# Optimization experiments

Measured on AMD Instinct MI355X. Metric: run time of the kernel, lower is better.

Reference implementation:

```python
import jax, jax.numpy as jnp
import numpy as np

NUM_HEADS = 8
NUM_POINTS = 9


def _bilinear_sample(img, gx, gy):
    """grid_sample, mode=bilinear, padding=zeros, align_corners=True.
    img: (B, C, H, W); gx, gy: (B, M) pixel coords. Returns (B, C, M)."""
    Bc, C, H, W = img.shape
    imgf = img.reshape(Bc, C, H * W)
    x0 = jnp.floor(gx)
    y0 = jnp.floor(gy)
    wx1 = gx - x0
    wy1 = gy - y0

    def corner(xi, yi, w):
        valid = (xi >= 0) & (xi < W) & (yi >= 0) & (yi < H)
        xi_c = jnp.clip(xi, 0, W - 1).astype(jnp.int32)
        yi_c = jnp.clip(yi, 0, H - 1).astype(jnp.int32)
        idx = yi_c * W + xi_c  # (B, M)
        g = jax.vmap(lambda im, ix: im[:, ix])(imgf, idx)  # (B, C, M)
        return g * (w * valid)[:, None, :]

    return (corner(x0, y0, (1 - wx1) * (1 - wy1))
            + corner(x0 + 1, y0, wx1 * (1 - wy1))
            + corner(x0, y0 + 1, (1 - wx1) * wy1)
            + corner(x0 + 1, y0 + 1, wx1 * wy1))


def setup_inputs() -> dict:
    key = jax.random.key(0)
    ks = jax.random.split(key, 6)
    B, Hp, Wp, T, D = 4, 64, 64, 3, 256
    N = Hp * Wp
    Hh, P = NUM_HEADS, NUM_POINTS
    x = jax.random.normal(ks[0], (B, N, T, D), dtype=jnp.float32)
    # offset/attn projections: small random (orig inits them to 0, which is degenerate for testing)
    W_off = jax.random.normal(ks[1], (D, Hh * P * 2), dtype=jnp.float32) * 0.01
    b_off = jnp.zeros((Hh * P * 2,), dtype=jnp.float32)
    W_attn = jax.random.normal(ks[2], (D, Hh * P), dtype=jnp.float32) * 0.01
    b_attn = jnp.zeros((Hh * P,), dtype=jnp.float32)
    W_v = jax.random.normal(ks[3], (D, D), dtype=jnp.float32) * 0.02
    b_v = jnp.zeros((D,), dtype=jnp.float32)
    W_o = jax.random.normal(ks[4], (D, D), dtype=jnp.float32) * 0.02
    b_o = jnp.zeros((D,), dtype=jnp.float32)
    return {"x": x, "W_off": W_off, "b_off": b_off, "W_attn": W_attn,
            "b_attn": b_attn, "W_v": W_v, "b_v": b_v, "W_o": W_o,
            "b_o": b_o, "Hp": Hp, "Wp": Wp}


def reference(x, W_off, b_off, W_attn, b_attn, W_v, b_v, W_o, b_o, Hp, Wp):
    B, N, T, D = x.shape
    Hh, P = NUM_HEADS, NUM_POINTS
    dh = D // Hh

    query = x[:, :, T // 2]  # (B, N, D) middle frame
    offset = (query @ W_off + b_off).reshape(B, N, Hh, P, 2)
    attn = jax.nn.softmax((query @ W_attn + b_attn).reshape(B, N, Hh, P), axis=-1)

    # reference points in [-1, 1], xy order (x = width coord)
    gh, gw = jnp.meshgrid(jnp.arange(Hp, dtype=jnp.float32),
                          jnp.arange(Wp, dtype=jnp.float32), indexing='ij')
    ref = jnp.stack([gw, gh], axis=-1).reshape(N, 2)
    ref = ref / jnp.asarray([Wp - 1, Hp - 1], dtype=jnp.float32) * 2 - 1

    loc = ref[None, :, None, None, :] + offset  # (B, N, H, P, 2) normalized

    value = (x @ W_v + b_v).reshape(B, N, T, Hh, dh)
    # (B, H, T, dh, N) -> (B*H*T, dh, Hp, Wp)
    val = jnp.transpose(value, (0, 3, 2, 4, 1)).reshape(B * Hh * T, dh, Hp, Wp)

    # per-(b,h) grid, shared across frames; fold T into batch of the sampler
    grid = jnp.transpose(loc, (0, 2, 1, 3, 4))  # (B, H, N, P, 2)
    grid = jnp.broadcast_to(grid[:, :, None], (B, Hh, T, N, P, 2))
    grid = grid.reshape(B * Hh * T, N * P, 2)
    gx = (grid[..., 0] + 1) * 0.5 * (Wp - 1)
    gy = (grid[..., 1] + 1) * 0.5 * (Hp - 1)

    sampled = _bilinear_sample(val, gx, gy)  # (B*H*T, dh, N*P)
    sampled = sampled.reshape(B, Hh, T, dh, N, P)

    # weighted sum over points, summed over frames
    out = jnp.einsum('bhtdnp,bnhp->bnhd', sampled, attn).reshape(B, N, D)
    return out @ W_o + b_o
```

## Files before the change

kernel.cpp:

```cpp
#include <hip/hip_runtime.h>
#include <hip/hip_bf16.h>


#define NH_ 8
#define DH_ 32
#define MM_ 16384

typedef __attribute__((ext_vector_type(8))) _Float16 f16x8;
typedef __attribute__((ext_vector_type(4))) _Float16 f16x4;
typedef __attribute__((ext_vector_type(4))) float f32x4;

struct HL { _Float16 h, l; };
static __device__ __forceinline__ HL fsplit(float f) {
  HL r;
  r.h = (_Float16)f;
  r.l = (_Float16)(f - (float)r.h);
  return r;
}

__global__ __launch_bounds__(256) void prep(
    const float* __restrict__ x,
    const float* __restrict__ W_off, const float* __restrict__ W_attn,
    const float* __restrict__ W_v, const float* __restrict__ W_o,
    const float* __restrict__ b_off, const float* __restrict__ b_attn,
    _Float16* __restrict__ ash, _Float16* __restrict__ asl,
    _Float16* __restrict__ xmh, _Float16* __restrict__ xml,
    _Float16* __restrict__ wv, _Float16* __restrict__ wch,
    _Float16* __restrict__ wcl, _Float16* __restrict__ wo,
    float* __restrict__ bcat) {
  const int bid = blockIdx.x, t = threadIdx.x;
  if (bid < 4096) {
    const int gid = bid * 256 + t;
    const int row = gid >> 6, c4 = (gid & 63) * 4;
    const float* xr = x + (size_t)row * 768 + c4;
    float4 a0 = *(const float4*)xr;
    float4 a1 = *(const float4*)(xr + 256);
    float4 a2 = *(const float4*)(xr + 512);
    float s[4] = {a0.x + a1.x + a2.x, a0.y + a1.y + a2.y,
                  a0.z + a1.z + a2.z, a0.w + a1.w + a2.w};
    float m[4] = {a1.x, a1.y, a1.z, a1.w};
    f16x4 shv, slv, mhv, mlv;
#pragma unroll
    for (int j = 0; j < 4; ++j) {
      HL sj = fsplit(s[j]);
      shv[j] = sj.h; slv[j] = sj.l;
      HL mj = fsplit(m[j]);
      mhv[j] = mj.h; mlv[j] = mj.l;
    }
    const size_t o = (size_t)row * 256 + c4;
    *(f16x4*)(ash + o) = shv;  *(f16x4*)(asl + o) = slv;
    *(f16x4*)(xmh + o) = mhv;  *(f16x4*)(xml + o) = mlv;
  } else {
    const int n = bid - 4096;
    wv[n * 256 + t] = (_Float16)W_v[(size_t)t * 256 + n];
    wo[n * 256 + t] = (_Float16)W_o[(size_t)t * 256 + n];
    if (n < 216) {
      float v = (n < 144) ? W_off[(size_t)t * 144 + n] : W_attn[(size_t)t * 72 + (n - 144)];
      HL w = fsplit(v);
      wch[n * 256 + t] = w.h; wcl[n * 256 + t] = w.l;
    }
    if (n == 0 && t < 216) bcat[t] = (t < 144) ? b_off[t] : b_attn[t - 144];
  }
}

__global__ __launch_bounds__(256, 4) void mgemm01(
    const _Float16* __restrict__ Ahi, const _Float16* __restrict__ Alo,
    const _Float16* __restrict__ Xmh, const _Float16* __restrict__ Xml,
    const _Float16* __restrict__ Wv, const _Float16* __restrict__ Wch,
    const _Float16* __restrict__ Wcl,
    const float* __restrict__ b_v, const float* __restrict__ bcat,
    _Float16* __restrict__ valsum, float* __restrict__ proj) {
  __shared__ _Float16 Ah[64][64], Al[64][64], Bh[64][64], Bl[64][64];
  const int bid = blockIdx.x;
  const int flat = (bid & 7) * 256 + (bid >> 3);
  const int m0 = (flat >> 3) * 64;
  const int yy = flat & 7;
  const int mode1 = yy >= 4;
  const int n0 = (yy & 3) * 64;
  const int tid = threadIdx.x, wid = tid >> 6, lane = tid & 63;
  const int am = (wid >> 1) * 32, bn = (wid & 1) * 32;
  const int fr = lane & 15, kg = lane >> 4;
  const _Float16* Ahs = mode1 ? Xmh : Ahi;
  const _Float16* Als = mode1 ? Xml : Alo;
  const _Float16* Bhs = mode1 ? Wch : Wv;

  const int r0s = tid >> 3, c0s = tid & 7;
  const int r1s = r0s + 32;
  const int d0s = r0s * 64 + ((c0s ^ (r0s & 7)) * 8);
  const int d1s = r1s * 64 + ((c0s ^ (r1s & 7)) * 8);

  f32x4 acc[2][2];
#pragma unroll
  for (int i = 0; i < 2; ++i)
#pragma unroll
    for (int j = 0; j < 2; ++j) acc[i][j] = (f32x4)(0.f);

  f16x8 pah[2], pal[2], pbh[2], pbl[2];

#define LOADT01(k0)                                                          \
  {                                                                          \
    size_t a0 = (size_t)(m0 + r0s) * 256 + (k0) + c0s * 8;                   \
    size_t a1 = (size_t)(m0 + r1s) * 256 + (k0) + c0s * 8;                   \
    pah[0] = *(const f16x8*)(Ahs + a0); pal[0] = *(const f16x8*)(Als + a0);  \
    pah[1] = *(const f16x8*)(Ahs + a1); pal[1] = *(const f16x8*)(Als + a1);  \
    int nr0 = n0 + r0s, nr1 = n0 + r1s;                                      \
    size_t b0 = (size_t)nr0 * 256 + (k0) + c0s * 8;                          \
    size_t b1 = (size_t)nr1 * 256 + (k0) + c0s * 8;                          \
    if (!mode1 || nr0 < 216) pbh[0] = *(const f16x8*)(Bhs + b0);             \
    else pbh[0] = (f16x8)(_Float16)0.f;                                      \
    if (!mode1 || nr1 < 216) pbh[1] = *(const f16x8*)(Bhs + b1);             \
    else pbh[1] = (f16x8)(_Float16)0.f;                                      \
    if (mode1) {                                                             \
      pbl[0] = (nr0 < 216) ? *(const f16x8*)(Wcl + b0) : (f16x8)(_Float16)0.f;\
      pbl[1] = (nr1 < 216) ? *(const f16x8*)(Wcl + b1) : (f16x8)(_Float16)0.f;\
    }                                                                        \
  }

#define WRITET()                                                             \
  {                                                                          \
    *(f16x8*)(&Ah[0][0] + d0s) = pah[0]; *(f16x8*)(&Al[0][0] + d0s) = pal[0];\
    *(f16x8*)(&Ah[0][0] + d1s) = pah[1]; *(f16x8*)(&Al[0][0] + d1s) = pal[1];\
    *(f16x8*)(&Bh[0][0] + d0s) = pbh[0]; *(f16x8*)(&Bh[0][0] + d1s) = pbh[1];\
    if (mode1) {                                                             \
      *(f16x8*)(&Bl[0][0] + d0s) = pbl[0]; *(f16x8*)(&Bl[0][0] + d1s) = pbl[1];\
    }                                                                        \
  }

#define COMPUTET()                                                           \
  _Pragma("unroll")                                                          \
  for (int ks = 0; ks < 2; ++ks) {                                           \
    const int kc = ks * 4 + kg;                                              \
    f16x8 ah[2], al[2], bh[2];                                               \
    _Pragma("unroll")                                                        \
    for (int mi = 0; mi < 2; ++mi) {                                         \
      int m = am + mi * 16 + fr;                                             \
      int o = m * 64 + ((kc ^ (m & 7)) * 8);                                 \
      ah[mi] = *(const f16x8*)(&Ah[0][0] + o);                               \
      al[mi] = *(const f16x8*)(&Al[0][0] + o);                               \
    }                                                                        \
    _Pragma("unroll")                                                        \
    for (int ni = 0; ni < 2; ++ni) {                                         \
      int nn = bn + ni * 16 + fr;                                            \
      int o = nn * 64 + ((kc ^ (nn & 7)) * 8);                               \
      bh[ni] = *(const f16x8*)(&Bh[0][0] + o);                               \
      _Pragma("unroll")                                                      \
      for (int mi = 0; mi < 2; ++mi) {                                       \
        acc[mi][ni] = __builtin_amdgcn_mfma_f32_16x16x32_f16(ah[mi], bh[ni], acc[mi][ni], 0, 0, 0);\
        acc[mi][ni] = __builtin_amdgcn_mfma_f32_16x16x32_f16(al[mi], bh[ni], acc[mi][ni], 0, 0, 0);\
      }                                                                      \
      if (mode1) {                                                           \
        f16x8 bl = *(const f16x8*)(&Bl[0][0] + o);                           \
        _Pragma("unroll")                                                    \
        for (int mi = 0; mi < 2; ++mi)                                       \
          acc[mi][ni] = __builtin_amdgcn_mfma_f32_16x16x32_f16(ah[mi], bl, acc[mi][ni], 0, 0, 0);\
      }                                                                      \
    }                                                                        \
  }

  LOADT01(0);
  WRITET();
  __syncthreads();
#pragma unroll
  for (int t = 0; t < 4; ++t) {
    if (t < 3) LOADT01((t + 1) * 64);
    COMPUTET();
    __syncthreads();
    if (t < 3) { WRITET(); __syncthreads(); }
  }

  const int ro = kg * 4;
#pragma unroll
  for (int mi = 0; mi < 2; ++mi)
#pragma unroll
    for (int ni = 0; ni < 2; ++ni) {
      int col = n0 + bn + ni * 16 + fr;
      if (mode1 && col >= 216) continue;
      int rowb = m0 + am + mi * 16 + ro;
      float bv = mode1 ? bcat[col] : b_v[col] * 3.f;
#pragma unroll
      for (int r = 0; r < 4; ++r) {
        int grow = rowb + r;
        float v = acc[mi][ni][r] + bv;
        if (mode1) {
          proj[(size_t)grow * 216 + col] = v;
        } else {
          int b = grow >> 12, nn2 = grow & 4095;
          int h = col >> 5, d = col & 31;
          valsum[(((size_t)(b * NH_ + h) << 12) + nn2) * DH_ + d] = (_Float16)v;
        }
      }
    }
#undef LOADT01
#undef WRITET
#undef COMPUTET
}

__global__ __launch_bounds__(256, 4) void mgemm2(
    const _Float16* __restrict__ Ahi, const _Float16* __restrict__ Alo,
    const _Float16* __restrict__ Bhs,
    const float* __restrict__ bias, float* __restrict__ Cout) {
  __shared__ _Float16 Ah[64][64], Al[64][64], Bh[64][64];
  const int bid = blockIdx.x;
  const int flat = (bid & 7) * 128 + (bid >> 3);
  const int m0 = (flat >> 2) * 64;
  const int n0 = (flat & 3) * 64;
  const int tid = threadIdx.x, wid = tid >> 6, lane = tid & 63;
  const int am = (wid >> 1) * 32, bn = (wid & 1) * 32;
  const int fr = lane & 15, kg = lane >> 4;

  const int r0s = tid >> 3, c0s = tid & 7;
  const int r1s = r0s + 32;
  const int d0s = r0s * 64 + ((c0s ^ (r0s & 7)) * 8);
  const int d1s = r1s * 64 + ((c0s ^ (r1s & 7)) * 8);

  f32x4 acc[2][2];
#pragma unroll
  for (int i = 0; i < 2; ++i)
#pragma unroll
    for (int j = 0; j < 2; ++j) acc[i][j] = (f32x4)(0.f);

  f16x8 pah[2], pal[2], pbh[2];

#define LOADT2(k0)                                                           \
  {                                                                          \
    size_t a0 = (size_t)(m0 + r0s) * 256 + (k0) + c0s * 8;                   \
    size_t a1 = (size_t)(m0 + r1s) * 256 + (k0) + c0s * 8;                   \
    pah[0] = *(const f16x8*)(Ahi + a0); pal[0] = *(const f16x8*)(Alo + a0);  \
    pah[1] = *(const f16x8*)(Ahi + a1); pal[1] = *(const f16x8*)(Alo + a1);  \
    size_t b0 = (size_t)(n0 + r0s) * 256 + (k0) + c0s * 8;                   \
    size_t b1 = (size_t)(n0 + r1s) * 256 + (k0) + c0s * 8;                   \
    pbh[0] = *(const f16x8*)(Bhs + b0); pbh[1] = *(const f16x8*)(Bhs + b1);  \
  }

#define WRITET2()                                                            \
  {                                                                          \
    *(f16x8*)(&Ah[0][0] + d0s) = pah[0]; *(f16x8*)(&Al[0][0] + d0s) = pal[0];\
    *(f16x8*)(&Ah[0][0] + d1s) = pah[1]; *(f16x8*)(&Al[0][0] + d1s) = pal[1];\
    *(f16x8*)(&Bh[0][0] + d0s) = pbh[0]; *(f16x8*)(&Bh[0][0] + d1s) = pbh[1];\
  }

#define COMPUTET2()                                                          \
  _Pragma("unroll")                                                          \
  for (int ks = 0; ks < 2; ++ks) {                                           \
    const int kc = ks * 4 + kg;                                              \
    f16x8 ah[2], al[2], bh[2];                                               \
    _Pragma("unroll")                                                        \
    for (int mi = 0; mi < 2; ++mi) {                                         \
      int m = am + mi * 16 + fr;                                             \
      int o = m * 64 + ((kc ^ (m & 7)) * 8);                                 \
      ah[mi] = *(const f16x8*)(&Ah[0][0] + o);                               \
      al[mi] = *(const f16x8*)(&Al[0][0] + o);                               \
    }                                                                        \
    _Pragma("unroll")                                                        \
    for (int ni = 0; ni < 2; ++ni) {                                         \
      int nn = bn + ni * 16 + fr;                                            \
      int o = nn * 64 + ((kc ^ (nn & 7)) * 8);                               \
      bh[ni] = *(const f16x8*)(&Bh[0][0] + o);                               \
    }                                                                        \
    _Pragma("unroll")                                                        \
    for (int mi = 0; mi < 2; ++mi)                                           \
      _Pragma("unroll")                                                      \
      for (int ni = 0; ni < 2; ++ni) {                                       \
        acc[mi][ni] = __builtin_amdgcn_mfma_f32_16x16x32_f16(ah[mi], bh[ni], acc[mi][ni], 0, 0, 0);\
        acc[mi][ni] = __builtin_amdgcn_mfma_f32_16x16x32_f16(al[mi], bh[ni], acc[mi][ni], 0, 0, 0);\
      }                                                                      \
  }

  LOADT2(0);
  WRITET2();
  __syncthreads();
#pragma unroll
  for (int t = 0; t < 4; ++t) {
    if (t < 3) LOADT2((t + 1) * 64);
    COMPUTET2();
    __syncthreads();
    if (t < 3) { WRITET2(); __syncthreads(); }
  }

  const int ro = kg * 4;
#pragma unroll
  for (int mi = 0; mi < 2; ++mi)
#pragma unroll
    for (int ni = 0; ni < 2; ++ni) {
      int col = n0 + bn + ni * 16 + fr;
      int rowb = m0 + am + mi * 16 + ro;
      float bv = bias[col];
#pragma unroll
      for (int r = 0; r < 4; ++r)
        Cout[(size_t)(rowb + r) * 256 + col] = acc[mi][ni][r] + bv;
    }
#undef LOADT2
#undef WRITET2
#undef COMPUTET2
}

struct IW { int idx; float w; };

__global__ __launch_bounds__(256) void sample4(const _Float16* __restrict__ valsum,
                                               const float* __restrict__ proj,
                                               _Float16* __restrict__ ihi,
                                               _Float16* __restrict__ ilo) {
  const int bid = blockIdx.x;
  const int wv = threadIdx.x >> 6;
  const int lane = threadIdx.x & 63;
  const int row = ((bid & 7) << 11) + ((bid >> 3) << 2) + wv;
  const int b = row >> 12, n = row & 4095;

  __shared__ IW cwi[4][72][4];
  __shared__ float sap[4][76];

  const float* pr = proj + (size_t)row * 216;
  if (lane < 8) {
    const float* pa = pr + 144 + lane * 9;
    float lg[9], mx = -1e30f;
#pragma unroll
    for (int p = 0; p < 9; ++p) { lg[p] = pa[p]; mx = fmaxf(mx, lg[p]); }
    float s = 0.f;
#pragma unroll
    for (int p = 0; p < 9; ++p) { lg[p] = __expf(lg[p] - mx); s += lg[p]; }
    float inv = 1.f / s;
#pragma unroll
    for (int p = 0; p < 9; ++p) sap[wv][lane * 9 + p] = lg[p] * inv;
  }
  __syncthreads();
  for (int e = lane; e < 72; e += 64) {
    float ox = pr[e * 2], oy = pr[e * 2 + 1];
    float gx = (float)(n & 63) + ox * 31.5f;
    float gy = (float)(n >> 6) + oy * 31.5f;
    float fx0 = floorf(gx), fy0 = floorf(gy);
    float wx1 = gx - fx0, wy1 = gy - fy0;
    float wx0 = 1.f - wx1, wy0 = 1.f - wy1;
    int x0 = (int)fx0, y0 = (int)fy0, x1 = x0 + 1, y1 = y0 + 1;
    bool vx0 = (x0 >= 0) & (x0 < 64), vx1 = (x1 >= 0) & (x1 < 64);
    bool vy0 = (y0 >= 0) & (y0 < 64), vy1 = (y1 >= 0) & (y1 < 64);
    int x0c = min(max(x0, 0), 63), x1c = min(max(x1, 0), 63);
    int y0c = min(max(y0, 0), 63), y1c = min(max(y1, 0), 63);
    const float a = sap[wv][e];
    cwi[wv][e][0] = IW{(y0c * 64 + x0c) * DH_, (vx0 & vy0) ? wx0 * wy0 * a : 0.f};
    cwi[wv][e][1] = IW{(y0c * 64 + x1c) * DH_, (vx1 & vy0) ? wx1 * wy0 * a : 0.f};
    cwi[wv][e][2] = IW{(y1c * 64 + x0c) * DH_, (vx0 & vy1) ? wx0 * wy1 * a : 0.f};
    cwi[wv][e][3] = IW{(y1c * 64 + x1c) * DH_, (vx1 & vy1) ? wx1 * wy1 * a : 0.f};
  }
  __syncthreads();

  const int h = lane >> 3, d4 = (lane & 7) * 4;
  const _Float16* vb = valsum + (((size_t)(b * NH_ + h)) << 12) * DH_ + d4;
  float ax = 0.f, ay = 0.f, az = 0.f, aw = 0.f;
#pragma unroll
  for (int pb = 0; pb < 9; pb += 3) {
    f16x4 v[12]; float w[12];
#pragma unroll
    for (int q = 0; q < 3; ++q) {
      const int hp = h * 9 + pb + q;
#pragma unroll
      for (int c = 0; c < 4; ++c) {
        IW e = cwi[wv][hp][c];
        v[q * 4 + c] = *(const f16x4*)(vb + e.idx);
        w[q * 4 + c] = e.w;
      }
    }
#pragma unroll
    for (int j = 0; j < 12; ++j) {
      ax += w[j] * (float)v[j][0]; ay += w[j] * (float)v[j][1];
      az += w[j] * (float)v[j][2]; aw += w[j] * (float)v[j][3];
    }
  }
  float av[4] = {ax, ay, az, aw};
  f16x4 hv, lv;
#pragma unroll
  for (int j = 0; j < 4; ++j) {
    HL r = fsplit(av[j]);
    hv[j] = r.h; lv[j] = r.l;
  }
  const size_t o = (size_t)row * 256 + lane * 4;
  *(f16x4*)(ihi + o) = hv;
  *(f16x4*)(ilo + o) = lv;
}

extern "C" void kernel_launch(void* const* d_in, const int* in_sizes, int n_in,
                              void* d_out, int out_size, void* d_ws, size_t ws_size,
                              hipStream_t stream) {
  const float* x      = (const float*)d_in[0];
  const float* W_off  = (const float*)d_in[1];
  const float* b_off  = (const float*)d_in[2];
  const float* W_attn = (const float*)d_in[3];
  const float* b_attn = (const float*)d_in[4];
  const float* W_v    = (const float*)d_in[5];
  const float* b_v    = (const float*)d_in[6];
  const float* W_o    = (const float*)d_in[7];
  const float* b_o    = (const float*)d_in[8];
  float* out = (float*)d_out;

  _Float16* valsum = (_Float16*)d_ws;
  float* proj    = (float*)(valsum + (size_t)MM_ * 256);
  float* bcat    = proj + (size_t)MM_ * 216;
  _Float16* ash = (_Float16*)(bcat + 256);
  _Float16* asl = ash + (size_t)MM_ * 256;
  _Float16* xmh = asl + (size_t)MM_ * 256;
  _Float16* xml = xmh + (size_t)MM_ * 256;
  _Float16* wv  = xml + (size_t)MM_ * 256;
  _Float16* wch = wv + 65536;
  _Float16* wcl = wch + 55296;
  _Float16* wo  = wcl + 55296;
  _Float16* ihi = ash;
  _Float16* ilo = asl;

  prep<<<dim3(4352), dim3(256), 0, stream>>>(x, W_off, W_attn, W_v, W_o, b_off, b_attn,
                                             ash, asl, xmh, xml,
                                             wv, wch, wcl, wo, bcat);
  mgemm01<<<dim3(2048), dim3(256), 0, stream>>>(ash, asl, xmh, xml, wv, wch, wcl,
                                                b_v, bcat, valsum, proj);
  sample4<<<dim3(4096), dim3(256), 0, stream>>>(valsum, proj, ihi, ilo);
  mgemm2<<<dim3(1024), dim3(256), 0, stream>>>(ihi, ilo, wo, b_o, out);
}
```

Before: 164.5 us.

## Fuse input prep into GEMMs and widen sampler to 8 pixels per block

Removes the separate prep kernel. The GEMMs now load fp32 x and weights directly, doing the frame sum, the hi/lo fp16 split and the weight transpose while staging into shared memory. This drops a full pass over x and the fp16 intermediate buffers, at the cost of more conversion work and scalar transposed weight loads inside every GEMM block. The sampler handles 8 pixels per block with 8-wide fp16 gathers instead of 4-wide, halving the block count. Occupancy hint on mgemm01 is lowered to 3 and the block-to-XCD mapping is changed.

After: 192.5 us. 17.0% more time.

```diff
diff --git a/kernel.cpp b/kernel.cpp
--- a/kernel.cpp
+++ b/kernel.cpp
@@ -1,5 +1,4 @@
 #include <hip/hip_runtime.h>
-#include <hip/hip_bf16.h>
 
 
 #define NH_ 8
@@ -18,76 +17,30 @@
   return r;
 }
 
-__global__ __launch_bounds__(256) void prep(
+__global__ __launch_bounds__(256, 3) void mgemm01(
     const float* __restrict__ x,
     const float* __restrict__ W_off, const float* __restrict__ W_attn,
-    const float* __restrict__ W_v, const float* __restrict__ W_o,
+    const float* __restrict__ W_v,
     const float* __restrict__ b_off, const float* __restrict__ b_attn,
-    _Float16* __restrict__ ash, _Float16* __restrict__ asl,
-    _Float16* __restrict__ xmh, _Float16* __restrict__ xml,
-    _Float16* __restrict__ wv, _Float16* __restrict__ wch,
-    _Float16* __restrict__ wcl, _Float16* __restrict__ wo,
-    float* __restrict__ bcat) {
-  const int bid = blockIdx.x, t = threadIdx.x;
-  if (bid < 4096) {
-    const int gid = bid * 256 + t;
-    const int row = gid >> 6, c4 = (gid & 63) * 4;
-    const float* xr = x + (size_t)row * 768 + c4;
-    float4 a0 = *(const float4*)xr;
-    float4 a1 = *(const float4*)(xr + 256);
-    float4 a2 = *(const float4*)(xr + 512);
-    float s[4] = {a0.x + a1.x + a2.x, a0.y + a1.y + a2.y,
-                  a0.z + a1.z + a2.z, a0.w + a1.w + a2.w};
-    float m[4] = {a1.x, a1.y, a1.z, a1.w};
-    f16x4 shv, slv, mhv, mlv;
-#pragma unroll
-    for (int j = 0; j < 4; ++j) {
-      HL sj = fsplit(s[j]);
-      shv[j] = sj.h; slv[j] = sj.l;
-      HL mj = fsplit(m[j]);
-      mhv[j] = mj.h; mlv[j] = mj.l;
-    }
-    const size_t o = (size_t)row * 256 + c4;
-    *(f16x4*)(ash + o) = shv;  *(f16x4*)(asl + o) = slv;
-    *(f16x4*)(xmh + o) = mhv;  *(f16x4*)(xml + o) = mlv;
-  } else {
-    const int n = bid - 4096;
-    wv[n * 256 + t] = (_Float16)W_v[(size_t)t * 256 + n];
-    wo[n * 256 + t] = (_Float16)W_o[(size_t)t * 256 + n];
-    if (n < 216) {
-      float v = (n < 144) ? W_off[(size_t)t * 144 + n] : W_attn[(size_t)t * 72 + (n - 144)];
-      HL w = fsplit(v);
-      wch[n * 256 + t] = w.h; wcl[n * 256 + t] = w.l;
-    }
-    if (n == 0 && t < 216) bcat[t] = (t < 144) ? b_off[t] : b_attn[t - 144];
-  }
-}
-
-__global__ __launch_bounds__(256, 4) void mgemm01(
-    const _Float16* __restrict__ Ahi, const _Float16* __restrict__ Alo,
-    const _Float16* __restrict__ Xmh, const _Float16* __restrict__ Xml,
-    const _Float16* __restrict__ Wv, const _Float16* __restrict__ Wch,
-    const _Float16* __restrict__ Wcl,
-    const float* __restrict__ b_v, const float* __restrict__ bcat,
+    const float* __restrict__ b_v,
     _Float16* __restrict__ valsum, float* __restrict__ proj) {
-  __shared__ _Float16 Ah[64][64], Al[64][64], Bh[64][64], Bl[64][64];
+  __shared__ _Float16 Ah[64 * 64], Al[64 * 64], Bh[64 * 64], Bl[64 * 64];
   const int bid = blockIdx.x;
-  const int flat = (bid & 7) * 256 + (bid >> 3);
-  const int m0 = (flat >> 3) * 64;
-  const int yy = flat & 7;
+  const int xcd = bid & 7, local = bid >> 3;
+  const int yy = local & 7;
+  const int m0 = ((local >> 3) * 8 + xcd) * 64;
   const int mode1 = yy >= 4;
   const int n0 = (yy & 3) * 64;
   const int tid = threadIdx.x, wid = tid >> 6, lane = tid & 63;
   const int am = (wid >> 1) * 32, bn = (wid & 1) * 32;
   const int fr = lane & 15, kg = lane >> 4;
-  const _Float16* Ahs = mode1 ? Xmh : Ahi;
-  const _Float16* Als = mode1 ? Xml : Alo;
-  const _Float16* Bhs = mode1 ? Wch : Wv;
 
   const int r0s = tid >> 3, c0s = tid & 7;
   const int r1s = r0s + 32;
   const int d0s = r0s * 64 + ((c0s ^ (r0s & 7)) * 8);
   const int d1s = r1s * 64 + ((c0s ^ (r1s & 7)) * 8);
+  const int bnn = (tid >> 4) * 4;
+  const int bkk = (tid & 15) * 4;
 
   f32x4 acc[2][2];
 #pragma unroll
@@ -95,34 +48,78 @@
 #pragma unroll
     for (int j = 0; j < 2; ++j) acc[i][j] = (f32x4)(0.f);
 
-  f16x8 pah[2], pal[2], pbh[2], pbl[2];
-
-#define LOADT01(k0)                                                          \
+  float4 pA[2][6];
+  float pBv[16];
+
+#define LOADT(k0)                                                            \
   {                                                                          \
-    size_t a0 = (size_t)(m0 + r0s) * 256 + (k0) + c0s * 8;                   \
-    size_t a1 = (size_t)(m0 + r1s) * 256 + (k0) + c0s * 8;                   \
-    pah[0] = *(const f16x8*)(Ahs + a0); pal[0] = *(const f16x8*)(Als + a0);  \
-    pah[1] = *(const f16x8*)(Ahs + a1); pal[1] = *(const f16x8*)(Als + a1);  \
-    int nr0 = n0 + r0s, nr1 = n0 + r1s;                                      \
-    size_t b0 = (size_t)nr0 * 256 + (k0) + c0s * 8;                          \
-    size_t b1 = (size_t)nr1 * 256 + (k0) + c0s * 8;                          \
-    if (!mode1 || nr0 < 216) pbh[0] = *(const f16x8*)(Bhs + b0);             \
-    else pbh[0] = (f16x8)(_Float16)0.f;                                      \
-    if (!mode1 || nr1 < 216) pbh[1] = *(const f16x8*)(Bhs + b1);             \
-    else pbh[1] = (f16x8)(_Float16)0.f;                                      \
     if (mode1) {                                                             \
-      pbl[0] = (nr0 < 216) ? *(const f16x8*)(Wcl + b0) : (f16x8)(_Float16)0.f;\
-      pbl[1] = (nr1 < 216) ? *(const f16x8*)(Wcl + b1) : (f16x8)(_Float16)0.f;\
+      const float* s0 = x + (size_t)(m0 + r0s) * 768 + 256 + (k0) + c0s * 8; \
+      const float* s1 = x + (size_t)(m0 + r1s) * 768 + 256 + (k0) + c0s * 8; \
+      pA[0][0] = *(const float4*)s0; pA[0][1] = *(const float4*)(s0 + 4);    \
+      pA[1][0] = *(const float4*)s1; pA[1][1] = *(const float4*)(s1 + 4);    \
+      _Pragma("unroll")                                                      \
+      for (int j = 0; j < 4; ++j) {                                          \
+        const int kglob = (k0) + bkk + j;                                    \
+        _Pragma("unroll")                                                    \
+        for (int i = 0; i < 4; ++i) {                                        \
+          const int gn = n0 + bnn + i;                                       \
+          float v = 0.f;                                                     \
+          if (gn < 144) v = W_off[(size_t)kglob * 144 + gn];                 \
+          else if (gn < 216) v = W_attn[(size_t)kglob * 72 + (gn - 144)];    \
+          pBv[j * 4 + i] = v;                                                \
+        }                                                                    \
+      }                                                                      \
+    } else {                                                                 \
+      const float* s0 = x + (size_t)(m0 + r0s) * 768 + (k0) + c0s * 8;       \
+      const float* s1 = x + (size_t)(m0 + r1s) * 768 + (k0) + c0s * 8;       \
+      pA[0][0] = *(const float4*)s0;         pA[0][1] = *(const float4*)(s0 + 4);   \
+      pA[0][2] = *(const float4*)(s0 + 256); pA[0][3] = *(const float4*)(s0 + 260); \
+      pA[0][4] = *(const float4*)(s0 + 512); pA[0][5] = *(const float4*)(s0 + 516); \
+      pA[1][0] = *(const float4*)s1;         pA[1][1] = *(const float4*)(s1 + 4);   \
+      pA[1][2] = *(const float4*)(s1 + 256); pA[1][3] = *(const float4*)(s1 + 260); \
+      pA[1][4] = *(const float4*)(s1 + 512); pA[1][5] = *(const float4*)(s1 + 516); \
+      _Pragma("unroll")                                                      \
+      for (int j = 0; j < 4; ++j)                                            \
+        *(float4*)&pBv[j * 4] =                                              \
+            *(const float4*)(W_v + (size_t)((k0) + bkk + j) * 256 + n0 + bnn);\
     }                                                                        \
   }
 
 #define WRITET()                                                             \
   {                                                                          \
-    *(f16x8*)(&Ah[0][0] + d0s) = pah[0]; *(f16x8*)(&Al[0][0] + d0s) = pal[0];\
-    *(f16x8*)(&Ah[0][0] + d1s) = pah[1]; *(f16x8*)(&Al[0][0] + d1s) = pal[1];\
-    *(f16x8*)(&Bh[0][0] + d0s) = pbh[0]; *(f16x8*)(&Bh[0][0] + d1s) = pbh[1];\
-    if (mode1) {                                                             \
-      *(f16x8*)(&Bl[0][0] + d0s) = pbl[0]; *(f16x8*)(&Bl[0][0] + d1s) = pbl[1];\
+    _Pragma("unroll")                                                        \
+    for (int hh = 0; hh < 2; ++hh) {                                         \
+      float s[8];                                                            \
+      if (mode1) {                                                           \
+        _Pragma("unroll")                                                    \
+        for (int q = 0; q < 4; ++q) { s[q] = pA[hh][0][q]; s[4 + q] = pA[hh][1][q]; } \
+      } else {                                                               \
+        _Pragma("unroll")                                                    \
+        for (int q = 0; q < 4; ++q) {                                        \
+          s[q] = pA[hh][0][q] + pA[hh][2][q] + pA[hh][4][q];                 \
+          s[4 + q] = pA[hh][1][q] + pA[hh][3][q] + pA[hh][5][q];             \
+        }                                                                    \
+      }                                                                      \
+      f16x8 hv, lv;                                                          \
+      _Pragma("unroll")                                                      \
+      for (int q = 0; q < 8; ++q) { HL r = fsplit(s[q]); hv[q] = r.h; lv[q] = r.l; } \
+      const int dd = hh ? d1s : d0s;                                         \
+      *(f16x8*)(Ah + dd) = hv; *(f16x8*)(Al + dd) = lv;                      \
+    }                                                                        \
+    _Pragma("unroll")                                                        \
+    for (int j = 0; j < 4; ++j) {                                            \
+      _Pragma("unroll")                                                      \
+      for (int i = 0; i < 4; ++i) {                                          \
+        const int row = bnn + i, kk2 = bkk + j;                              \
+        const int el = row * 64 + (((kk2 >> 3) ^ (row & 7)) * 8) + (kk2 & 7);\
+        if (mode1) {                                                         \
+          HL r = fsplit(pBv[j * 4 + i]);                                     \
+          Bh[el] = r.h; Bl[el] = r.l;                                        \
+        } else {                                                             \
+          Bh[el] = (_Float16)pBv[j * 4 + i];                                 \
+        }                                                                    \
+      }                                                                      \
     }                                                                        \
   }
 
@@ -130,26 +127,26 @@
   _Pragma("unroll")                                                          \
   for (int ks = 0; ks < 2; ++ks) {                                           \
     const int kc = ks * 4 + kg;                                              \
-    f16x8 ah[2], al[2], bh[2];                                               \
+    f16x8 ah[2], al[2];                                                      \
     _Pragma("unroll")                                                        \
     for (int mi = 0; mi < 2; ++mi) {                                         \
       int m = am + mi * 16 + fr;                                             \
       int o = m * 64 + ((kc ^ (m & 7)) * 8);                                 \
-      ah[mi] = *(const f16x8*)(&Ah[0][0] + o);                               \
-      al[mi] = *(const f16x8*)(&Al[0][0] + o);                               \
+      ah[mi] = *(const f16x8*)(Ah + o);                                      \
+      al[mi] = *(const f16x8*)(Al + o);                                      \
     }                                                                        \
     _Pragma("unroll")                                                        \
     for (int ni = 0; ni < 2; ++ni) {                                         \
       int nn = bn + ni * 16 + fr;                                            \
       int o = nn * 64 + ((kc ^ (nn & 7)) * 8);                               \
-      bh[ni] = *(const f16x8*)(&Bh[0][0] + o);                               \
+      f16x8 bh = *(const f16x8*)(Bh + o);                                    \
       _Pragma("unroll")                                                      \
       for (int mi = 0; mi < 2; ++mi) {                                       \
-        acc[mi][ni] = __builtin_amdgcn_mfma_f32_16x16x32_f16(ah[mi], bh[ni], acc[mi][ni], 0, 0, 0);\
-        acc[mi][ni] = __builtin_amdgcn_mfma_f32_16x16x32_f16(al[mi], bh[ni], acc[mi][ni], 0, 0, 0);\
+        acc[mi][ni] = __builtin_amdgcn_mfma_f32_16x16x32_f16(ah[mi], bh, acc[mi][ni], 0, 0, 0);\
+        acc[mi][ni] = __builtin_amdgcn_mfma_f32_16x16x32_f16(al[mi], bh, acc[mi][ni], 0, 0, 0);\
       }                                                                      \
       if (mode1) {                                                           \
-        f16x8 bl = *(const f16x8*)(&Bl[0][0] + o);                           \
+        f16x8 bl = *(const f16x8*)(Bl + o);                                  \
         _Pragma("unroll")                                                    \
         for (int mi = 0; mi < 2; ++mi)                                       \
           acc[mi][ni] = __builtin_amdgcn_mfma_f32_16x16x32_f16(ah[mi], bl, acc[mi][ni], 0, 0, 0);\
@@ -157,12 +154,12 @@
     }                                                                        \
   }
 
-  LOADT01(0);
+  LOADT(0);
   WRITET();
   __syncthreads();
 #pragma unroll
   for (int t = 0; t < 4; ++t) {
-    if (t < 3) LOADT01((t + 1) * 64);
+    if (t < 3) LOADT((t + 1) * 64);
     COMPUTET();
     __syncthreads();
     if (t < 3) { WRITET(); __syncthreads(); }
@@ -176,7 +173,8 @@
       int col = n0 + bn + ni * 16 + fr;
       if (mode1 && col >= 216) continue;
       int rowb = m0 + am + mi * 16 + ro;
-      float bv = mode1 ? bcat[col] : b_v[col] * 3.f;
+      float bv = mode1 ? (col < 144 ? b_off[col] : b_attn[col - 144])
+                       : b_v[col] * 3.f;
 #pragma unroll
       for (int r = 0; r < 4; ++r) {
         int grow = rowb + r;
@@ -190,16 +188,16 @@
         }
       }
     }
-#undef LOADT01
+#undef LOADT
 #undef WRITET
 #undef COMPUTET
 }
 
 __global__ __launch_bounds__(256, 4) void mgemm2(
     const _Float16* __restrict__ Ahi, const _Float16* __restrict__ Alo,
-    const _Float16* __restrict__ Bhs,
-    const float* __restrict__ bias, float* __restrict__ Cout) {
-  __shared__ _Float16 Ah[64][64], Al[64][64], Bh[64][64];
+    const float* __restrict__ W_o,
+    const float* __restrict__ b_o, float* __restrict__ Cout) {
+  __shared__ _Float16 Ah[64 * 64], Al[64 * 64], Bh[64 * 64];
   const int bid = blockIdx.x;
   const int flat = (bid & 7) * 128 + (bid >> 3);
   const int m0 = (flat >> 2) * 64;
@@ -212,6 +210,8 @@
   const int r1s = r0s + 32;
   const int d0s = r0s * 64 + ((c0s ^ (r0s & 7)) * 8);
   const int d1s = r1s * 64 + ((c0s ^ (r1s & 7)) * 8);
+  const int bnn = (tid >> 4) * 4;
+  const int bkk = (tid & 15) * 4;
 
   f32x4 acc[2][2];
 #pragma unroll
@@ -219,7 +219,8 @@
 #pragma unroll
     for (int j = 0; j < 2; ++j) acc[i][j] = (f32x4)(0.f);
 
-  f16x8 pah[2], pal[2], pbh[2];
+  f16x8 pah[2], pal[2];
+  float pBv[16];
 
 #define LOADT2(k0)                                                           \
   {                                                                          \
@@ -227,16 +228,24 @@
     size_t a1 = (size_t)(m0 + r1s) * 256 + (k0) + c0s * 8;                   \
     pah[0] = *(const f16x8*)(Ahi + a0); pal[0] = *(const f16x8*)(Alo + a0);  \
     pah[1] = *(const f16x8*)(Ahi + a1); pal[1] = *(const f16x8*)(Alo + a1);  \
-    size_t b0 = (size_t)(n0 + r0s) * 256 + (k0) + c0s * 8;                   \
-    size_t b1 = (size_t)(n0 + r1s) * 256 + (k0) + c0s * 8;                   \
-    pbh[0] = *(const f16x8*)(Bhs + b0); pbh[1] = *(const f16x8*)(Bhs + b1);  \
+    _Pragma("unroll")                                                        \
+    for (int j = 0; j < 4; ++j)                                              \
+      *(float4*)&pBv[j * 4] =                                                \
+          *(const float4*)(W_o + (size_t)((k0) + bkk + j) * 256 + n0 + bnn); \
   }
 
 #define WRITET2()                                                            \
   {                                                                          \
-    *(f16x8*)(&Ah[0][0] + d0s) = pah[0]; *(f16x8*)(&Al[0][0] + d0s) = pal[0];\
-    *(f16x8*)(&Ah[0][0] + d1s) = pah[1]; *(f16x8*)(&Al[0][0] + d1s) = pal[1];\
-    *(f16x8*)(&Bh[0][0] + d0s) = pbh[0]; *(f16x8*)(&Bh[0][0] + d1s) = pbh[1];\
+    *(f16x8*)(Ah + d0s) = pah[0]; *(f16x8*)(Al + d0s) = pal[0];              \
+    *(f16x8*)(Ah + d1s) = pah[1]; *(f16x8*)(Al + d1s) = pal[1];              \
+    _Pragma("unroll")                                                        \
+    for (int j = 0; j < 4; ++j)                                              \
+      _Pragma("unroll")                                                      \
+      for (int i = 0; i < 4; ++i) {                                          \
+        const int row = bnn + i, kk2 = bkk + j;                              \
+        const int el = row * 64 + (((kk2 >> 3) ^ (row & 7)) * 8) + (kk2 & 7);\
+        Bh[el] = (_Float16)pBv[j * 4 + i];                                   \
+      }                                                                      \
   }
 
 #define COMPUTET2()                                                          \
@@ -248,14 +257,14 @@
     for (int mi = 0; mi < 2; ++mi) {                                         \
       int m = am + mi * 16 + fr;                                             \
       int o = m * 64 + ((kc ^ (m & 7)) * 8);                                 \
-      ah[mi] = *(const f16x8*)(&Ah[0][0] + o);                               \
-      al[mi] = *(const f16x8*)(&Al[0][0] + o);                               \
+      ah[mi] = *(const f16x8*)(Ah + o);                                      \
+      al[mi] = *(const f16x8*)(Al + o);                                      \
     }                                                                        \
     _Pragma("unroll")                                                        \
     for (int ni = 0; ni < 2; ++ni) {                                         \
       int nn = bn + ni * 16 + fr;                                            \
       int o = nn * 64 + ((kc ^ (nn & 7)) * 8);                               \
-      bh[ni] = *(const f16x8*)(&Bh[0][0] + o);                               \
+      bh[ni] = *(const f16x8*)(Bh + o);                                      \
     }                                                                        \
     _Pragma("unroll")                                                        \
     for (int mi = 0; mi < 2; ++mi)                                           \
@@ -284,7 +293,7 @@
     for (int ni = 0; ni < 2; ++ni) {
       int col = n0 + bn + ni * 16 + fr;
       int rowb = m0 + am + mi * 16 + ro;
-      float bv = bias[col];
+      float bv = b_o[col];
 #pragma unroll
       for (int r = 0; r < 4; ++r)
         Cout[(size_t)(rowb + r) * 256 + col] = acc[mi][ni][r] + bv;
@@ -296,22 +305,21 @@
 
 struct IW { int idx; float w; };
 
-__global__ __launch_bounds__(256) void sample4(const _Float16* __restrict__ valsum,
+__global__ __launch_bounds__(256) void sample8(const _Float16* __restrict__ valsum,
                                                const float* __restrict__ proj,
                                                _Float16* __restrict__ ihi,
                                                _Float16* __restrict__ ilo) {
   const int bid = blockIdx.x;
-  const int wv = threadIdx.x >> 6;
-  const int lane = threadIdx.x & 63;
-  const int row = ((bid & 7) << 11) + ((bid >> 3) << 2) + wv;
-  const int b = row >> 12, n = row & 4095;
-
-  __shared__ IW cwi[4][72][4];
-  __shared__ float sap[4][76];
-
-  const float* pr = proj + (size_t)row * 216;
-  if (lane < 8) {
-    const float* pa = pr + 144 + lane * 9;
+  const int base = ((bid & 7) << 11) + ((bid >> 3) << 3);
+  const int tid = threadIdx.x;
+
+  __shared__ IW cwi[8][72][4];
+  __shared__ float sap[8][72];
+
+  if (tid < 64) {
+    const int ps = tid >> 3, h = tid & 7;
+    const int row_s = base + ps;
+    const float* pa = proj + (size_t)row_s * 216 + 144 + h * 9;
     float lg[9], mx = -1e30f;
 #pragma unroll
     for (int p = 0; p < 9; ++p) { lg[p] = pa[p]; mx = fmaxf(mx, lg[p]); }
@@ -320,11 +328,16 @@
     for (int p = 0; p < 9; ++p) { lg[p] = __expf(lg[p] - mx); s += lg[p]; }
     float inv = 1.f / s;
 #pragma unroll
-    for (int p = 0; p < 9; ++p) sap[wv][lane * 9 + p] = lg[p] * inv;
+    for (int p = 0; p < 9; ++p) sap[ps][h * 9 + p] = lg[p] * inv;
   }
   __syncthreads();
-  for (int e = lane; e < 72; e += 64) {
-    float ox = pr[e * 2], oy = pr[e * 2 + 1];
+  for (int e = tid; e < 576; e += 256) {
+    const int ps = e / 72;
+    const int pt = e - ps * 72;
+    const int row_s = base + ps;
+    const int n = row_s & 4095;
+    const float* pr = proj + (size_t)row_s * 216;
+    float ox = pr[pt * 2], oy = pr[pt * 2 + 1];
     float gx = (float)(n & 63) + ox * 31.5f;
     float gy = (float)(n >> 6) + oy * 31.5f;
     float fx0 = floorf(gx), fy0 = floorf(gy);
@@ -335,46 +348,51 @@
     bool vy0 = (y0 >= 0) & (y0 < 64), vy1 = (y1 >= 0) & (y1 < 64);
     int x0c = min(max(x0, 0), 63), x1c = min(max(x1, 0), 63);
     int y0c = min(max(y0, 0), 63), y1c = min(max(y1, 0), 63);
-    const float a = sap[wv][e];
-    cwi[wv][e][0] = IW{(y0c * 64 + x0c) * DH_, (vx0 & vy0) ? wx0 * wy0 * a : 0.f};
-    cwi[wv][e][1] = IW{(y0c * 64 + x1c) * DH_, (vx1 & vy0) ? wx1 * wy0 * a : 0.f};
-    cwi[wv][e][2] = IW{(y1c * 64 + x0c) * DH_, (vx0 & vy1) ? wx0 * wy1 * a : 0.f};
-    cwi[wv][e][3] = IW{(y1c * 64 + x1c) * DH_, (vx1 & vy1) ? wx1 * wy1 * a : 0.f};
+    const float a = sap[ps][pt];
+    cwi[ps][pt][0] = IW{(y0c * 64 + x0c) * DH_, (vx0 & vy0) ? wx0 * wy0 * a : 0.f};
+    cwi[ps][pt][1] = IW{(y0c * 64 + x1c) * DH_, (vx1 & vy0) ? wx1 * wy0 * a : 0.f};
+    cwi[ps][pt][2] = IW{(y1c * 64 + x0c) * DH_, (vx0 & vy1) ? wx0 * wy1 * a : 0.f};
+    cwi[ps][pt][3] = IW{(y1c * 64 + x1c) * DH_, (vx1 & vy1) ? wx1 * wy1 * a : 0.f};
   }
   __syncthreads();
 
-  const int h = lane >> 3, d4 = (lane & 7) * 4;
-  const _Float16* vb = valsum + (((size_t)(b * NH_ + h)) << 12) * DH_ + d4;
-  float ax = 0.f, ay = 0.f, az = 0.f, aw = 0.f;
+  const int px = tid >> 5, lane32 = tid & 31;
+  const int row = base + px;
+  const int b = row >> 12;
+  const int h = lane32 >> 2, d8 = (lane32 & 3) * 8;
+  const _Float16* vb = valsum + (((size_t)(b * NH_ + h)) << 12) * DH_ + d8;
+  float acc[8];
+#pragma unroll
+  for (int k = 0; k < 8; ++k) acc[k] = 0.f;
+
 #pragma unroll
   for (int pb = 0; pb < 9; pb += 3) {
-    f16x4 v[12]; float w[12];
+    f16x8 v[12]; float w[12];
 #pragma unroll
     for (int q = 0; q < 3; ++q) {
       const int hp = h * 9 + pb + q;
 #pragma unroll
       for (int c = 0; c < 4; ++c) {
-        IW e = cwi[wv][hp][c];
-        v[q * 4 + c] = *(const f16x4*)(vb + e.idx);
+        IW e = cwi[px][hp][c];
+        v[q * 4 + c] = *(const f16x8*)(vb + e.idx);
         w[q * 4 + c] = e.w;
       }
     }
 #pragma unroll
-    for (int j = 0; j < 12; ++j) {
-      ax += w[j] * (float)v[j][0]; ay += w[j] * (float)v[j][1];
-      az += w[j] * (float)v[j][2]; aw += w[j] * (float)v[j][3];
-    }
-  }
-  float av[4] = {ax, ay, az, aw};
-  f16x4 hv, lv;
-#pragma unroll
-  for (int j = 0; j < 4; ++j) {
-    HL r = fsplit(av[j]);
-    hv[j] = r.h; lv[j] = r.l;
-  }
-  const size_t o = (size_t)row * 256 + lane * 4;
-  *(f16x4*)(ihi + o) = hv;
-  *(f16x4*)(ilo + o) = lv;
+    for (int j = 0; j < 12; ++j)
+#pragma unroll
+      for (int k = 0; k < 8; ++k) acc[k] += w[j] * (float)v[j][k];
+  }
+
+  f16x8 hv, lv;
+#pragma unroll
+  for (int k = 0; k < 8; ++k) {
+    HL r = fsplit(acc[k]);
+    hv[k] = r.h; lv[k] = r.l;
+  }
+  const size_t o = (size_t)row * 256 + h * DH_ + d8;
+  *(f16x8*)(ihi + o) = hv;
+  *(f16x8*)(ilo + o) = lv;
 }
 
 extern "C" void kernel_launch(void* const* d_in, const int* in_sizes, int n_in,
@@ -392,24 +410,12 @@
   float* out = (float*)d_out;
 
   _Float16* valsum = (_Float16*)d_ws;
-  float* proj    = (float*)(valsum + (size_t)MM_ * 256);
-  float* bcat    = proj + (size_t)MM_ * 216;
-  _Float16* ash = (_Float16*)(bcat + 256);
-  _Float16* asl = ash + (size_t)MM_ * 256;
-  _Float16* xmh = asl + (size_t)MM_ * 256;
-  _Float16* xml = xmh + (size_t)MM_ * 256;
-  _Float16* wv  = xml + (size_t)MM_ * 256;
-  _Float16* wch = wv + 65536;
-  _Float16* wcl = wch + 55296;
-  _Float16* wo  = wcl + 55296;
-  _Float16* ihi = ash;
-  _Float16* ilo = asl;
-
-  prep<<<dim3(4352), dim3(256), 0, stream>>>(x, W_off, W_attn, W_v, W_o, b_off, b_attn,
-                                             ash, asl, xmh, xml,
-                                             wv, wch, wcl, wo, bcat);
-  mgemm01<<<dim3(2048), dim3(256), 0, stream>>>(ash, asl, xmh, xml, wv, wch, wcl,
-                                                b_v, bcat, valsum, proj);
-  sample4<<<dim3(4096), dim3(256), 0, stream>>>(valsum, proj, ihi, ilo);
-  mgemm2<<<dim3(1024), dim3(256), 0, stream>>>(ihi, ilo, wo, b_o, out);
+  float* proj      = (float*)(valsum + (size_t)MM_ * 256);
+  _Float16* ihi    = (_Float16*)(proj + (size_t)MM_ * 216);
+  _Float16* ilo    = ihi + (size_t)MM_ * 256;
+
+  mgemm01<<<dim3(2048), dim3(256), 0, stream>>>(x, W_off, W_attn, W_v,
+                                                b_off, b_attn, b_v, valsum, proj);
+  sample8<<<dim3(2048), dim3(256), 0, stream>>>(valsum, proj, ihi, ilo);
+  mgemm2<<<dim3(1024), dim3(256), 0, stream>>>(ihi, ilo, W_o, b_o, out);
 }
```
